# Optimization experiments

Measured on AMD Instinct MI355X. Metric: run time of the kernel, lower is better.

Reference implementation:

```python
import jax, jax.numpy as jnp
import numpy as np

jax.config.update("jax_enable_x64", True)  # scipy.special.expi computes in float64; match it internally

_GAMMA = 0.5772156649015328606  # Euler-Mascheroni constant
_SERIES_TERMS = 120   # power series: accurate for |x| <= 40 in float64
_ASYM_TERMS = 30      # asymptotic series for x >= 40
_CF_DEPTH = 60        # continued fraction for E1(z), z >= 6
_X_HI = 40.0
_X_LO = -6.0


def _ei_series(x):
    # Ei(x) = gamma + ln|x| + sum_{n>=1} x^n / (n * n!)
    def body(carry, n):
        t, s = carry
        t = t * x / n          # t_n = x^n / n!
        return (t, s + t / n), None
    ns = jnp.arange(1.0, _SERIES_TERMS + 1.0, dtype=x.dtype)
    (_, s), _ = jax.lax.scan(body, (jnp.ones_like(x), jnp.zeros_like(x)), ns)
    return _GAMMA + jnp.log(jnp.abs(x)) + s


def _ei_asymptotic(x):
    # Ei(x) ~ e^x / x * sum_{k>=0} k! / x^k   (x large positive)
    def body(carry, k):
        t, s = carry
        t = t * k / x          # t_k = k! / x^k
        return (t, s + t), None
    ks = jnp.arange(1.0, _ASYM_TERMS + 1.0, dtype=x.dtype)
    (_, s), _ = jax.lax.scan(body, (jnp.ones_like(x), jnp.ones_like(x)), ks)
    return jnp.exp(x) / x * s


def _e1_cf(z):
    # E1(z) = e^{-z} / (z + 1 - 1/(z + 3 - 4/(z + 5 - 9/(...))))  (z > 0)
    def body(i, f):
        k = _CF_DEPTH - i      # k runs _CF_DEPTH .. 1
        return z + 2.0 * k - 1.0 - (k * k) / f
    f0 = z + 2.0 * _CF_DEPTH + 1.0
    f = jax.lax.fori_loop(0, _CF_DEPTH, body, f0)
    return jnp.exp(-z) / f


def _ei_impl(x):
    xs = x.astype(jnp.float64)
    ser = _ei_series(jnp.clip(xs, _X_LO, _X_HI))
    asy = _ei_asymptotic(jnp.maximum(xs, _X_HI))
    neg = -_e1_cf(jnp.maximum(-xs, -_X_LO))   # Ei(x) = -E1(-x) for x < 0
    out = jnp.where(xs >= _X_HI, asy, jnp.where(xs <= _X_LO, neg, ser))
    return out.astype(x.dtype)


@jax.custom_vjp
def ei(x):
    return _ei_impl(x)


def _ei_fwd(x):
    return _ei_impl(x), x


def _ei_bwd(x, g):
    # matches the torch module's custom backward: d/dx Ei(x) = e^x / x
    return (g * jnp.exp(x) / x,)


ei.defvjp(_ei_fwd, _ei_bwd)


def setup_inputs() -> dict:
    key = jax.random.key(0)
    # scale by 20 so all three Ei domains (series / neg continued fraction / asymptotic) are hit
    x = jax.random.normal(key, (8192, 4096), dtype=jnp.float32) * 20.0
    return {"x": x}


def reference(x):
    return ei(x)
```

## Files before the change

### kernel.cpp

```cpp
#include <hip/hip_runtime.h>
#include <math.h>


static constexpr double cexp(double x) {
    double t = x * 1.4426950408889634074;
    long long n = (long long)(t + (t >= 0 ? 0.5 : -0.5));
    double r = x - (double)n * 0.693147180559945286227e0;
    r -= (double)n * 2.319046813846299558e-17;
    double s = 1.0, term = 1.0;
    for (int k = 1; k <= 22; ++k) { term = term * r / (double)k; s += term; }
    double p = 1.0, b = 2.0;
    long long m = n < 0 ? -n : n;
    while (m) { if (m & 1) p *= b; b *= b; m >>= 1; }
    return n < 0 ? s / p : s * p;
}
static constexpr double clog(double x) {
    int e = 0; double m = x;
    while (m > 1.4142135623730951) { m *= 0.5; ++e; }
    while (m < 0.7071067811865476) { m *= 2.0; --e; }
    double t = (m - 1.0) / (m + 1.0), t2 = t * t, s = 0.0, p = t;
    for (int k = 0; k < 14; ++k) { s += p / (double)(2 * k + 1); p *= t2; }
    return 2.0 * s + (double)e * 0.69314718055994530942;
}
static constexpr double f_value(double x) {
    if (x <= -6.0) {
        double z = -x;
        double f = z + 121.0;
        for (int k = 60; k >= 1; --k)
            f = z + 2.0 * (double)k - 1.0 - ((double)k * (double)k) / f;
        return -1.0 / f;
    } else if (x >= 40.0) {
        double u = 1.0 / x, s = 1.0, t = 1.0;
        for (int k = 1; k <= 30; ++k) { t = t * (double)k * u; s += t; }
        return u * s;
    } else {
        double t = 1.0, s = 0.0;
        for (int n = 1; n <= 120; ++n) { t = t * x / (double)n; s += t / (double)n; }
        double Ei = 0.57721566490153286061 + clog(x < 0.0 ? -x : x) + s;
        return Ei * cexp(-x);
    }
}
static constexpr double S_coeff(double x, int k) {
    double sum = 0.0, nf = 1.0;
    for (int n = 1; n <= 45; ++n) {
        nf *= (double)n;
        if (n >= k) {
            double c = 1.0;
            for (int t = 0; t < k; ++t) c = c * (double)(n - t) / (double)(t + 1);
            double xp = 1.0;
            for (int t = 0; t < n - k; ++t) xp *= x;
            sum += c * xp / ((double)n * nf);
        }
    }
    return sum;
}

struct Chunk { alignas(16) float c[256][4]; };
static constexpr Chunk make_chunk(int base) {
    Chunk ch{};
    for (int i = 0; i < 256; ++i) {
        double xj = -128.0 + 0.0625 * (double)(base + i);
        if (xj > -0.95 && xj < 0.95) {
            for (int k = 0; k < 4; ++k) ch.c[i][k] = (float)S_coeff(xj, k);
        } else {
            double fk = f_value(xj);
            ch.c[i][0] = (float)fk;
            double fact = 1.0, xp = 1.0, kf = 1.0;
            for (int k = 1; k <= 3; ++k) {
                if (k >= 2) fact *= (double)(k - 1);
                xp *= xj;
                fk = ((k & 1) ? fact : -fact) / xp - fk;
                kf *= (double)k;
                ch.c[i][k] = (float)(fk / kf);
            }
        }
    }
    return ch;
}
static constexpr Chunk g_c0  = make_chunk(0);    static constexpr Chunk g_c1  = make_chunk(256);
static constexpr Chunk g_c2  = make_chunk(512);  static constexpr Chunk g_c3  = make_chunk(768);
static constexpr Chunk g_c4  = make_chunk(1024); static constexpr Chunk g_c5  = make_chunk(1280);
static constexpr Chunk g_c6  = make_chunk(1536); static constexpr Chunk g_c7  = make_chunk(1792);
static constexpr Chunk g_c8  = make_chunk(2048); static constexpr Chunk g_c9  = make_chunk(2304);
static constexpr Chunk g_c10 = make_chunk(2560); static constexpr Chunk g_c11 = make_chunk(2816);
static constexpr Chunk g_c12 = make_chunk(3072); static constexpr Chunk g_c13 = make_chunk(3328);
static constexpr Chunk g_c14 = make_chunk(3584); static constexpr Chunk g_c15 = make_chunk(3840);
__device__ const Chunk g_tab[16] = {g_c0,g_c1,g_c2,g_c3,g_c4,g_c5,g_c6,g_c7,
                                    g_c8,g_c9,g_c10,g_c11,g_c12,g_c13,g_c14,g_c15};

__device__ __forceinline__ float ei_one(float xf, const float4* s_tab) {
    int j = (int)rintf(fmaf(xf, 16.0f, 2048.0f));
    j = j < 0 ? 0 : (j > 4095 ? 4095 : j);
    float4 c = s_tab[j];
    float xj = fmaf(0.0625f, (float)j, -128.0f);
    float d = xf - xj;
    float s = fmaf(fmaf(fmaf(c.w, d, c.z), d, c.y), d, c.x);
    float nf = rintf(xf * 1.44269504f);
    float rr = fmaf(nf, -0.693145751953125f, xf);
    rr = fmaf(nf, -1.42860677e-6f, rr);
    float rA = ldexpf(exp2f(rr * 1.44269504f) * s, (int)nf);
    float rB = fmaf(0.69314718f, log2f(fabsf(xf)), 0.57721566f) + s;
    float r = (j > 2032 && j < 2064) ? rB : rA;
    if (!(r == r)) r = 0.0f;
    return fminf(fmaxf(r, -3.3e38f), 3.3e38f);
}

__global__ __launch_bounds__(1024)
void ei_kernel(const float* __restrict__ x, float* __restrict__ out, int n) {
    __shared__ float4 s_tab[4096];
    const float4* gt = (const float4*)g_tab;
    #pragma unroll
    for (int t = 0; t < 4; ++t)
        s_tab[threadIdx.x + 1024 * t] = gt[threadIdx.x + 1024 * t];
    __syncthreads();

    int n4 = n >> 2;
    int stride = gridDim.x * blockDim.x;
    for (int q = blockIdx.x * blockDim.x + threadIdx.x; q < n4; q += stride) {
        int base = q * 4;
        float4 xv = *(const float4*)(x + base);
        float4 o;
        o.x = ei_one(xv.x, s_tab);
        o.y = ei_one(xv.y, s_tab);
        o.z = ei_one(xv.z, s_tab);
        o.w = ei_one(xv.w, s_tab);
        *(float4*)(out + base) = o;
    }
    if (blockIdx.x == 0 && threadIdx.x == 0) {
        for (int t = n & ~3; t < n; ++t) out[t] = ei_one(x[t], s_tab);
    }
}

extern "C" void kernel_launch(void* const* d_in, const int* in_sizes, int n_in,
                              void* d_out, int out_size, void* d_ws, size_t ws_size,
                              hipStream_t stream) {
    const float* x = (const float*)d_in[0];
    float* out = (float*)d_out;
    int n = in_sizes[0];
    const int block = 1024;
    const int grid = 512;
    ei_kernel<<<grid, block, 0, stream>>>(x, out, n);
}
```

Before: 232.4 us.

## Software-pipeline global loads two iterations ahead and use nontemporal output stores

Restructures the grid-stride loop to prefetch the next two float4 input vectors while the current two are computed. All four LDS table lookups for a float4 are issued before any polynomial evaluation. Output is written with nontemporal stores, and launch bounds now request 8 waves per EU occupancy. The aim is to hide HBM latency on this memory-bound kernel, at the cost of more live registers. Split scalar nontemporal stores may not coalesce as well as one float4 store.

```diff
diff --git a/kernel.cpp b/kernel.cpp
--- a/kernel.cpp
+++ b/kernel.cpp
@@ -88,10 +88,15 @@
 __device__ const Chunk g_tab[16] = {g_c0,g_c1,g_c2,g_c3,g_c4,g_c5,g_c6,g_c7,
                                     g_c8,g_c9,g_c10,g_c11,g_c12,g_c13,g_c14,g_c15};
 
-__device__ __forceinline__ float ei_one(float xf, const float4* s_tab) {
+__device__ __forceinline__ void ei_prep(float xf, const float4* s_tab,
+                                        int& jo, float4& co) {
     int j = (int)rintf(fmaf(xf, 16.0f, 2048.0f));
     j = j < 0 ? 0 : (j > 4095 ? 4095 : j);
-    float4 c = s_tab[j];
+    jo = j;
+    co = s_tab[j];
+}
+
+__device__ __forceinline__ float ei_finish(float xf, int j, float4 c) {
     float xj = fmaf(0.0625f, (float)j, -128.0f);
     float d = xf - xj;
     float s = fmaf(fmaf(fmaf(c.w, d, c.z), d, c.y), d, c.x);
@@ -100,12 +105,27 @@
     rr = fmaf(nf, -1.42860677e-6f, rr);
     float rA = ldexpf(exp2f(rr * 1.44269504f) * s, (int)nf);
     float rB = fmaf(0.69314718f, log2f(fabsf(xf)), 0.57721566f) + s;
-    float r = (j > 2032 && j < 2064) ? rB : rA;
+    float r = ((unsigned)(j - 2033) < 31u) ? rB : rA;
     if (!(r == r)) r = 0.0f;
     return fminf(fmaxf(r, -3.3e38f), 3.3e38f);
 }
 
-__global__ __launch_bounds__(1024)
+__device__ __forceinline__ float4 ei4(float4 xv, const float4* s_tab) {
+    int j0, j1, j2, j3;
+    float4 c0, c1, c2, c3;
+    ei_prep(xv.x, s_tab, j0, c0);
+    ei_prep(xv.y, s_tab, j1, c1);
+    ei_prep(xv.z, s_tab, j2, c2);
+    ei_prep(xv.w, s_tab, j3, c3);
+    float4 o;
+    o.x = ei_finish(xv.x, j0, c0);
+    o.y = ei_finish(xv.y, j1, c1);
+    o.z = ei_finish(xv.z, j2, c2);
+    o.w = ei_finish(xv.w, j3, c3);
+    return o;
+}
+
+__global__ __launch_bounds__(1024, 8)
 void ei_kernel(const float* __restrict__ x, float* __restrict__ out, int n) {
     __shared__ float4 s_tab[4096];
     const float4* gt = (const float4*)g_tab;
@@ -114,20 +134,48 @@
         s_tab[threadIdx.x + 1024 * t] = gt[threadIdx.x + 1024 * t];
     __syncthreads();
 
-    int n4 = n >> 2;
-    int stride = gridDim.x * blockDim.x;
-    for (int q = blockIdx.x * blockDim.x + threadIdx.x; q < n4; q += stride) {
-        int base = q * 4;
-        float4 xv = *(const float4*)(x + base);
-        float4 o;
-        o.x = ei_one(xv.x, s_tab);
-        o.y = ei_one(xv.y, s_tab);
-        o.z = ei_one(xv.z, s_tab);
-        o.w = ei_one(xv.w, s_tab);
-        *(float4*)(out + base) = o;
+    const int n4 = n >> 2;
+    const int stride = gridDim.x * blockDim.x;
+
+    int qa = blockIdx.x * blockDim.x + threadIdx.x;
+    int qb = qa + stride;
+    bool va = qa < n4, vb = qb < n4;
+    float4 xa, xb;
+    if (va) xa = *(const float4*)(x + 4 * qa);
+    if (vb) xb = *(const float4*)(x + 4 * qb);
+
+    while (va) {
+        int qc = qb + stride, qd = qc + stride;
+        bool vc = qc < n4, vd = qd < n4;
+        float4 xc, xd;
+        if (vc) xc = *(const float4*)(x + 4 * qc);
+        if (vd) xd = *(const float4*)(x + 4 * qd);
+
+        {
+            float4 o = ei4(xa, s_tab);
+            __builtin_nontemporal_store(o.x, out + 4 * qa + 0);
+            __builtin_nontemporal_store(o.y, out + 4 * qa + 1);
+            __builtin_nontemporal_store(o.z, out + 4 * qa + 2);
+            __builtin_nontemporal_store(o.w, out + 4 * qa + 3);
+        }
+        if (vb) {
+            float4 o = ei4(xb, s_tab);
+            __builtin_nontemporal_store(o.x, out + 4 * qb + 0);
+            __builtin_nontemporal_store(o.y, out + 4 * qb + 1);
+            __builtin_nontemporal_store(o.z, out + 4 * qb + 2);
+            __builtin_nontemporal_store(o.w, out + 4 * qb + 3);
+        }
+
+        qa = qc; va = vc; xa = xc;
+        qb = qd; vb = vd; xb = xd;
     }
+
     if (blockIdx.x == 0 && threadIdx.x == 0) {
-        for (int t = n & ~3; t < n; ++t) out[t] = ei_one(x[t], s_tab);
+        for (int t = n & ~3; t < n; ++t) {
+            int j; float4 c;
+            ei_prep(x[t], s_tab, j, c);
+            out[t] = ei_finish(x[t], j, c);
+        }
     }
 }
 
```

Result: slower. 237.2 us (+2.1%).

## Software-pipeline loads, split LUT into float2 planes, use native exp2/log2

Applied to the files above, without the earlier changes.

Adds an exact-trip-count kernel that prefetches the next pair of float4 inputs while computing the current eight elements, and writes results with nontemporal stores. The shared-memory coefficient table is split into two float2 planes, and the NaN check is dropped. exp2f/log2f are replaced by native OCML approximations, and launch bounds request higher occupancy. This targets memory latency and transcendental cost, at the risk of slightly lower accuracy from the native exp/log and of NaN inputs now propagating.

```diff
diff --git a/kernel.cpp b/kernel.cpp
--- a/kernel.cpp
+++ b/kernel.cpp
@@ -1,6 +1,11 @@
 #include <hip/hip_runtime.h>
 #include <math.h>
 
+
+typedef float f32x4_t __attribute__((ext_vector_type(4)));
+
+extern "C" __device__ float __ocml_native_exp2_f32(float) __attribute__((const));
+extern "C" __device__ float __ocml_native_log2_f32(float) __attribute__((const));
 
 static constexpr double cexp(double x) {
     double t = x * 1.4426950408889634074;
@@ -88,46 +93,128 @@
 __device__ const Chunk g_tab[16] = {g_c0,g_c1,g_c2,g_c3,g_c4,g_c5,g_c6,g_c7,
                                     g_c8,g_c9,g_c10,g_c11,g_c12,g_c13,g_c14,g_c15};
 
-__device__ __forceinline__ float ei_one(float xf, const float4* s_tab) {
+__device__ __forceinline__ void ei_prep(float xf, const float2* s2,
+                                        int& jo, float2& ab, float2& cd) {
     int j = (int)rintf(fmaf(xf, 16.0f, 2048.0f));
     j = j < 0 ? 0 : (j > 4095 ? 4095 : j);
-    float4 c = s_tab[j];
+    jo = j;
+    ab = s2[j];
+    cd = s2[j + 4096];
+}
+
+__device__ __forceinline__ float ei_finish(float xf, int j, float2 ab, float2 cd) {
     float xj = fmaf(0.0625f, (float)j, -128.0f);
     float d = xf - xj;
-    float s = fmaf(fmaf(fmaf(c.w, d, c.z), d, c.y), d, c.x);
+    float s = fmaf(fmaf(fmaf(cd.y, d, cd.x), d, ab.y), d, ab.x);
     float nf = rintf(xf * 1.44269504f);
     float rr = fmaf(nf, -0.693145751953125f, xf);
     rr = fmaf(nf, -1.42860677e-6f, rr);
-    float rA = ldexpf(exp2f(rr * 1.44269504f) * s, (int)nf);
-    float rB = fmaf(0.69314718f, log2f(fabsf(xf)), 0.57721566f) + s;
-    float r = (j > 2032 && j < 2064) ? rB : rA;
-    if (!(r == r)) r = 0.0f;
+    float rA = ldexpf(__ocml_native_exp2_f32(rr * 1.44269504f) * s, (int)nf);
+    float rB = fmaf(0.69314718f, __ocml_native_log2_f32(fabsf(xf)), 0.57721566f) + s;
+    float r = ((unsigned)(j - 2033) < 31u) ? rB : rA;
     return fminf(fmaxf(r, -3.3e38f), 3.3e38f);
 }
 
-__global__ __launch_bounds__(1024)
-void ei_kernel(const float* __restrict__ x, float* __restrict__ out, int n) {
-    __shared__ float4 s_tab[4096];
+__device__ __forceinline__ void nt_store4(float* p, float4 v) {
+    f32x4_t t; t.x = v.x; t.y = v.y; t.z = v.z; t.w = v.w;
+    __builtin_nontemporal_store(t, (f32x4_t*)p);
+}
+
+__device__ __forceinline__ void ei8(float4 xa, float4 xb, const float2* s2,
+                                    float4& oa, float4& ob) {
+    int j0, j1, j2, j3, j4, j5, j6, j7;
+    float2 a0, a1, a2, a3, a4, a5, a6, a7;
+    float2 b0, b1, b2, b3, b4, b5, b6, b7;
+    ei_prep(xa.x, s2, j0, a0, b0);
+    ei_prep(xa.y, s2, j1, a1, b1);
+    ei_prep(xa.z, s2, j2, a2, b2);
+    ei_prep(xa.w, s2, j3, a3, b3);
+    ei_prep(xb.x, s2, j4, a4, b4);
+    ei_prep(xb.y, s2, j5, a5, b5);
+    ei_prep(xb.z, s2, j6, a6, b6);
+    ei_prep(xb.w, s2, j7, a7, b7);
+    oa.x = ei_finish(xa.x, j0, a0, b0);
+    oa.y = ei_finish(xa.y, j1, a1, b1);
+    oa.z = ei_finish(xa.z, j2, a2, b2);
+    oa.w = ei_finish(xa.w, j3, a3, b3);
+    ob.x = ei_finish(xb.x, j4, a4, b4);
+    ob.y = ei_finish(xb.y, j5, a5, b5);
+    ob.z = ei_finish(xb.z, j6, a6, b6);
+    ob.w = ei_finish(xb.w, j7, a7, b7);
+}
+
+__device__ __forceinline__ void stage_table(float2* s2) {
     const float4* gt = (const float4*)g_tab;
     #pragma unroll
-    for (int t = 0; t < 4; ++t)
-        s_tab[threadIdx.x + 1024 * t] = gt[threadIdx.x + 1024 * t];
+    for (int t = 0; t < 4; ++t) {
+        int idx = threadIdx.x + 1024 * t;
+        float4 c = gt[idx];
+        float2 lo; lo.x = c.x; lo.y = c.y;
+        float2 hi; hi.x = c.z; hi.y = c.w;
+        s2[idx] = lo;
+        s2[idx + 4096] = hi;
+    }
     __syncthreads();
+}
+
+__global__ __launch_bounds__(1024, 8)
+void ei_kernel_exact(const float* __restrict__ x, float* __restrict__ out,
+                     int iters) {
+    __shared__ float2 s_tab2[8192];
+    stage_table(s_tab2);
+
+    const int S = gridDim.x * blockDim.x;
+    int qa = blockIdx.x * blockDim.x + threadIdx.x;
+    int qb = qa + S;
+    float4 xa = *(const float4*)(x + 4 * qa);
+    float4 xb = *(const float4*)(x + 4 * qb);
+
+    for (int it = 0; it < iters - 2; it += 2) {
+        float4 xc = *(const float4*)(x + 4 * (qa + 2 * S));
+        float4 xd = *(const float4*)(x + 4 * (qb + 2 * S));
+
+        float4 oa, ob;
+        ei8(xa, xb, s_tab2, oa, ob);
+        nt_store4(out + 4 * qa, oa);
+        nt_store4(out + 4 * qb, ob);
+
+        qa += 2 * S; qb += 2 * S;
+        xa = xc; xb = xd;
+    }
+    float4 oa, ob;
+    ei8(xa, xb, s_tab2, oa, ob);
+    nt_store4(out + 4 * qa, oa);
+    nt_store4(out + 4 * qb, ob);
+}
+
+__global__ __launch_bounds__(1024, 8)
+void ei_kernel_generic(const float* __restrict__ x, float* __restrict__ out, int n) {
+    __shared__ float2 s_tab2[8192];
+    stage_table(s_tab2);
 
     int n4 = n >> 2;
     int stride = gridDim.x * blockDim.x;
     for (int q = blockIdx.x * blockDim.x + threadIdx.x; q < n4; q += stride) {
-        int base = q * 4;
-        float4 xv = *(const float4*)(x + base);
+        float4 xv = *(const float4*)(x + 4 * q);
+        int j0, j1, j2, j3;
+        float2 a0, a1, a2, a3, b0, b1, b2, b3;
+        ei_prep(xv.x, s_tab2, j0, a0, b0);
+        ei_prep(xv.y, s_tab2, j1, a1, b1);
+        ei_prep(xv.z, s_tab2, j2, a2, b2);
+        ei_prep(xv.w, s_tab2, j3, a3, b3);
         float4 o;
-        o.x = ei_one(xv.x, s_tab);
-        o.y = ei_one(xv.y, s_tab);
-        o.z = ei_one(xv.z, s_tab);
-        o.w = ei_one(xv.w, s_tab);
-        *(float4*)(out + base) = o;
+        o.x = ei_finish(xv.x, j0, a0, b0);
+        o.y = ei_finish(xv.y, j1, a1, b1);
+        o.z = ei_finish(xv.z, j2, a2, b2);
+        o.w = ei_finish(xv.w, j3, a3, b3);
+        *(float4*)(out + 4 * q) = o;
     }
     if (blockIdx.x == 0 && threadIdx.x == 0) {
-        for (int t = n & ~3; t < n; ++t) out[t] = ei_one(x[t], s_tab);
+        for (int t = n & ~3; t < n; ++t) {
+            int j; float2 a, b;
+            ei_prep(x[t], s_tab2, j, a, b);
+            out[t] = ei_finish(x[t], j, a, b);
+        }
     }
 }
 
@@ -139,5 +226,12 @@
     int n = in_sizes[0];
     const int block = 1024;
     const int grid = 512;
-    ei_kernel<<<grid, block, 0, stream>>>(x, out, n);
-}
+    long long T = (long long)grid * block;
+    int n4 = n >> 2;
+    long long it = (n & 3) == 0 && n4 % T == 0 ? n4 / T : 0;
+    if (it >= 4 && (it & 1) == 0) {
+        ei_kernel_exact<<<grid, block, 0, stream>>>(x, out, (int)it);
+    } else {
+        ei_kernel_generic<<<grid, block, 0, stream>>>(x, out, n);
+    }
+}
```

New measurement: 234.8 us. No clear change (+1.0%).
